# Kernel tuning notes

Hardware: AMD Instinct MI355X
Metric: run time of the kernel (lower is better)

## Reference

```python
import jax, jax.numpy as jnp
import numpy as np

B, F, L, P, H = 32, 64, 8192, 96, 8
HD = F // H
EPS_ATTN = 1e-6
EPS_REVIN = 1e-5
EPS_LN = 1e-5


def setup_inputs() -> dict:
    key = jax.random.key(0)
    ks = jax.random.split(key, 8)
    f32 = jnp.float32
    return {
        'x': jax.random.normal(ks[0], (B, F, L), dtype=f32),
        'gamma': jnp.ones((1, 1, F), dtype=f32),
        'beta': jnp.zeros((1, 1, F), dtype=f32),
        'ln_w': jnp.ones((F,), dtype=f32),
        'ln_b': jnp.zeros((F,), dtype=f32),
        'Wq': 0.05 * jax.random.normal(ks[1], (F, F), dtype=f32),
        'bq': jnp.zeros((F,), dtype=f32),
        'Wk': 0.05 * jax.random.normal(ks[2], (F, F), dtype=f32),
        'bk': jnp.zeros((F,), dtype=f32),
        'Wv': 0.05 * jax.random.normal(ks[3], (F, F), dtype=f32),
        'bv': jnp.zeros((F,), dtype=f32),
        'Wo': 0.05 * jax.random.normal(ks[4], (F, F), dtype=f32),
        'bo': jnp.zeros((F,), dtype=f32),
        'Wlin': 0.01 * jax.random.normal(ks[5], (P, L), dtype=f32),
        'blin': jnp.zeros((P,), dtype=f32),
        'Wp': 0.1 * jax.random.normal(ks[6], (1, F), dtype=f32),
        'bp': jnp.zeros((1,), dtype=f32),
    }


def _phi(t):
    # feature map: elu(x) + 1 (non-negative)
    return jax.nn.elu(t) + 1.0


def _layernorm(h, w, b):
    mu = jnp.mean(h, axis=-1, keepdims=True)
    var = jnp.mean(jnp.square(h - mu), axis=-1, keepdims=True)
    return (h - mu) * jax.lax.rsqrt(var + EPS_LN) * w + b


def reference(x, gamma, beta, ln_w, ln_b, Wq, bq, Wk, bk, Wv, bv, Wo, bo,
              Wlin, blin, Wp, bp):
    # (B, F, L) -> (B, L, F)
    xt = jnp.transpose(x, (0, 2, 1))
    # RevIN norm (stats over time axis, detached; torch std is unbiased ddof=1)
    mean = jax.lax.stop_gradient(jnp.mean(xt, axis=1, keepdims=True))
    std = jax.lax.stop_gradient(jnp.std(xt, axis=1, keepdims=True, ddof=1) + EPS_REVIN)
    xn = (xt - mean) / std * gamma + beta
    residual = xn
    h = _layernorm(xn, ln_w, ln_b)
    # Q/K/V projections (torch Linear: h @ W.T + b)
    Q = h @ Wq.T + bq
    K = h @ Wk.T + bk
    V = h @ Wv.T + bv
    # (B, L, F) -> (B, H, L, HD)
    def heads(t):
        return jnp.transpose(t.reshape(B, L, H, HD), (0, 2, 1, 3))
    Q, K, V = heads(Q), heads(K), heads(V)
    Q, K = _phi(Q), _phi(K)
    # linear attention: phi(Q) (phi(K)^T V) / (phi(Q) sum_n phi(K))
    KV = jnp.einsum('bhnd,bhne->bhde', K, V)           # (B,H,HD,HD)
    out = jnp.einsum('bhnd,bhde->bhne', Q, KV)          # (B,H,L,HD)
    Z = jnp.sum(K, axis=2)                              # (B,H,HD)
    normalizer = jnp.einsum('bhnd,bhd->bhn', Q, Z)[..., None] + EPS_ATTN
    out = out / normalizer
    out = jnp.transpose(out, (0, 2, 1, 3)).reshape(B, L, F)
    out = out @ Wo.T + bo
    y = out + residual                                  # (B, L, F)
    # temporal linear: (B, F, L) @ Wlin.T -> (B, F, P) -> (B, P, F)
    y = jnp.transpose(jnp.transpose(y, (0, 2, 1)) @ Wlin.T + blin, (0, 2, 1))
    # RevIN denorm
    y = (y - beta) / gamma
    y = y * std + mean
    # projector to scalar per step
    return (y @ Wp.T + bp)[..., 0]                      # (B, P)
```

## Files before the change

kernel.cpp:

```cpp
#include <hip/hip_runtime.h>
#include <cstddef>

#define NB 32
#define NF 64
#define NL 8192
#define NP 96
#define NH 8
#define TSPLIT 16

#define WS_MEAN 0
#define WS_STD  2048
#define WS_RSTD 4096
#define WS_KV   6144
#define WS_Z    22528
#define WS_OUT2 24576
#define WS_MUN  221184
#define WS_RSN  483328
#define WS_WLB  745472
#define WS_XNB  1138688
#define WS_YT   9527296
#define WS_WKV  17915904
#define WS_WQO  17920512
#define WS_SKT  17925120
#define WS_SQT  17925376

typedef __bf16 bfx8 __attribute__((ext_vector_type(8)));
typedef float f32x4 __attribute__((ext_vector_type(4)));
#define MFMA16(a, b, c) __builtin_amdgcn_mfma_f32_16x16x32_bf16((a), (b), (c), 0, 0, 0)

__device__ __forceinline__ unsigned short f2bf(float f) {
  unsigned u = __float_as_uint(f);
  unsigned r = u + 0x7FFFu + ((u >> 16) & 1u);
  return (unsigned short)(r >> 16);
}
__device__ __forceinline__ unsigned packbf2(float lo, float hi) {
  return (unsigned)f2bf(lo) | ((unsigned)f2bf(hi) << 16);
}
__device__ __forceinline__ float bflo(unsigned d) { return __uint_as_float(d << 16); }
__device__ __forceinline__ float bfhi(unsigned d) { return __uint_as_float(d & 0xFFFF0000u); }
__device__ __forceinline__ float bf1(unsigned short s) { return __uint_as_float(((unsigned)s) << 16); }

__device__ __forceinline__ bfx8 ldfrag(const unsigned short* p) {
  uint4 u = *(const uint4*)p;
  return __builtin_bit_cast(bfx8, u);
}

__global__ __launch_bounds__(256) void k_pre(
    const float* __restrict__ x, const float* __restrict__ Wlin,
    const float* __restrict__ lnw, const float* __restrict__ lnb,
    const float* __restrict__ Wk, const float* __restrict__ bk,
    const float* __restrict__ Wv, const float* __restrict__ bv,
    const float* __restrict__ Wq, const float* __restrict__ bq,
    const float* __restrict__ Wo,
    float* __restrict__ wmean, float* __restrict__ wstd, float* __restrict__ wrstd,
    unsigned short* __restrict__ wlb, float* __restrict__ zz,
    unsigned short* __restrict__ wWkv, unsigned short* __restrict__ wWqo,
    float* __restrict__ wSkT, float* __restrict__ wSqT) {
  __shared__ float r1[4], r2[4];
  const int bid = blockIdx.x, tid = threadIdx.x;
  if (bid < NB * NF) {
    const float4* row4 = (const float4*)(x + (size_t)bid * NL);
    float s1 = 0.f, s2 = 0.f;
#pragma unroll
    for (int i = 0; i < NL / 4 / 256; i++) {
      float4 v = row4[tid + i * 256];
      s1 += v.x + v.y + v.z + v.w;
      s2 += v.x * v.x + v.y * v.y + v.z * v.z + v.w * v.w;
    }
#pragma unroll
    for (int off = 32; off > 0; off >>= 1) {
      s1 += __shfl_down(s1, off, 64);
      s2 += __shfl_down(s2, off, 64);
    }
    if ((tid & 63) == 0) { r1[tid >> 6] = s1; r2[tid >> 6] = s2; }
    __syncthreads();
    if (tid == 0) {
      s1 = r1[0] + r1[1] + r1[2] + r1[3];
      s2 = r2[0] + r2[1] + r2[2] + r2[3];
      float m = s1 * (1.f / NL);
      float var = (s2 - (float)NL * m * m) * (1.f / (NL - 1));
      float sd = sqrtf(fmaxf(var, 0.f)) + 1e-5f;
      wmean[bid] = m;
      wstd[bid] = sd;
      wrstd[bid] = 1.f / sd;
    }
    unsigned zi = (unsigned)bid * 256u + (unsigned)tid;
    if (zi < 215040u) zz[zi] = 0.f;
  } else if (bid < NB * NF + NP * NL / 8 / 256) {
    int i = (bid - NB * NF) * 256 + tid;
    int p = i >> 10;
    int l8 = (i & 1023) * 8;
    float4 va = *(const float4*)&Wlin[(size_t)p * NL + l8];
    float4 vb = *(const float4*)&Wlin[(size_t)p * NL + l8 + 4];
    uint4 o;
    o.x = packbf2(va.x, va.y); o.y = packbf2(va.z, va.w);
    o.z = packbf2(vb.x, vb.y); o.w = packbf2(vb.z, vb.w);
    *(uint4*)&wlb[(((size_t)(l8 >> 5)) * NP + p) * 32 + (l8 & 31)] = o;
  } else if (bid == NB * NF + NP * NL / 8 / 256) {
    int jj = tid >> 2, g = tid & 3;
    int f0 = g * 16;
    float tkp = 0.f, tvp = 0.f, skp = 0.f, svp = 0.f;
#pragma unroll
    for (int i = 0; i < 4; i++) {
      int f = f0 + i * 4;
      float4 wk4 = *(const float4*)&Wk[jj * NF + f];
      float4 wv4 = *(const float4*)&Wv[jj * NF + f];
      float4 lw  = *(const float4*)&lnw[f];
      float4 lb  = *(const float4*)&lnb[f];
      uint2 pk2, pv2;
      pk2.x = packbf2(wk4.x * lw.x, wk4.y * lw.y);
      pk2.y = packbf2(wk4.z * lw.z, wk4.w * lw.w);
      pv2.x = packbf2(wv4.x * lw.x, wv4.y * lw.y);
      pv2.y = packbf2(wv4.z * lw.z, wv4.w * lw.w);
      *(uint2*)&wWkv[jj * 72 + f] = pk2;
      *(uint2*)&wWkv[4608 + jj * 72 + f] = pv2;
      tkp += lb.x * wk4.x + lb.y * wk4.y + lb.z * wk4.z + lb.w * wk4.w;
      tvp += lb.x * wv4.x + lb.y * wv4.y + lb.z * wv4.z + lb.w * wv4.w;
      skp += bflo(pk2.x) + bfhi(pk2.x) + bflo(pk2.y) + bfhi(pk2.y);
      svp += bflo(pv2.x) + bfhi(pv2.x) + bflo(pv2.y) + bfhi(pv2.y);
    }
    tkp += __shfl_xor(tkp, 1, 64); tkp += __shfl_xor(tkp, 2, 64);
    tvp += __shfl_xor(tvp, 1, 64); tvp += __shfl_xor(tvp, 2, 64);
    skp += __shfl_xor(skp, 1, 64); skp += __shfl_xor(skp, 2, 64);
    svp += __shfl_xor(svp, 1, 64); svp += __shfl_xor(svp, 2, 64);
    if (g == 0) {
      wSkT[jj]       = skp;
      wSkT[64 + jj]  = tkp + bk[jj];
      wSkT[128 + jj] = svp;
      wSkT[192 + jj] = tvp + bv[jj];
    }
  } else {
    int jj = tid >> 2, g = tid & 3;
    int f0 = g * 16;
    float tqp = 0.f, sqp = 0.f;
#pragma unroll
    for (int i = 0; i < 4; i++) {
      int f = f0 + i * 4;
      float4 wq4 = *(const float4*)&Wq[jj * NF + f];
      float4 wo4 = *(const float4*)&Wo[jj * NF + f];
      float4 lw  = *(const float4*)&lnw[f];
      float4 lb  = *(const float4*)&lnb[f];
      uint2 pq2, po2;
      pq2.x = packbf2(wq4.x * lw.x, wq4.y * lw.y);
      pq2.y = packbf2(wq4.z * lw.z, wq4.w * lw.w);
      po2.x = packbf2(wo4.x, wo4.y);
      po2.y = packbf2(wo4.z, wo4.w);
      *(uint2*)&wWqo[jj * 72 + f] = pq2;
      *(uint2*)&wWqo[4608 + jj * 72 + f] = po2;
      tqp += lb.x * wq4.x + lb.y * wq4.y + lb.z * wq4.z + lb.w * wq4.w;
      sqp += bflo(pq2.x) + bfhi(pq2.x) + bflo(pq2.y) + bfhi(pq2.y);
    }
    tqp += __shfl_xor(tqp, 1, 64); tqp += __shfl_xor(tqp, 2, 64);
    sqp += __shfl_xor(sqp, 1, 64); sqp += __shfl_xor(sqp, 2, 64);
    if (g == 0) { wSqT[jj] = sqp; wSqT[64 + jj] = tqp + bq[jj]; }
  }
}

__global__ __launch_bounds__(256, 4) void k_kv(
    const float* __restrict__ x,
    const float* __restrict__ gamma, const float* __restrict__ beta,
    const unsigned short* __restrict__ wWkv, const float* __restrict__ wSkT,
    const float* __restrict__ wmean, const float* __restrict__ wrstd,
    float* __restrict__ wKV, float* __restrict__ wZ,
    float* __restrict__ wmun, float* __restrict__ wrsn,
    unsigned short* __restrict__ xnb) {
  __shared__ __align__(16) char smem[39424];
  unsigned short* hA  = (unsigned short*)smem;
  unsigned short* WkB = (unsigned short*)(smem + 18432);
  unsigned short* WvB = (unsigned short*)(smem + 27648);
  unsigned short* pK  = (unsigned short*)smem;
  unsigned short* pV  = (unsigned short*)(smem + 17408);
  float* SkT  = (float*)(smem + 36864);
  float* mun  = (float*)(smem + 37888);
  float* rsn  = (float*)(smem + 38400);
  float* cbc  = (float*)(smem + 38912);

  const int tid = threadIdx.x;
  const int b = blockIdx.x >> 6;
  const int tI = blockIdx.x & 63;
  const int L0 = tI * 128;
  const int lane = tid & 63, wv = tid >> 6;
  const int mm = lane & 15, qd = lane >> 4;

  if (tid < 64) {
    float cb = wrstd[b * NF + tid] * gamma[tid];
    cbc[2 * tid] = cb;
    cbc[2 * tid + 1] = beta[tid] - wmean[b * NF + tid] * cb;
  }
  {
    uint4* dst = (uint4*)(smem + 18432);
    const uint4* src = (const uint4*)wWkv;
#pragma unroll
    for (int i = 0; i < 4; i++) dst[tid + i * 256] = src[tid + i * 256];
    if (tid < 128) dst[tid + 1024] = src[tid + 1024];
    SkT[tid] = wSkT[tid];
  }
  __syncthreads();

  {
    const int lt = tid >> 3;
    const int fg = tid & 7;
    const int l0q = lt * 4;
    const float* xp = x + ((size_t)(b * NF + fg * 8)) * NL + L0 + l0q;
    f32x4 v[8];
#pragma unroll
    for (int i = 0; i < 8; i++) v[i] = *(const f32x4*)(xp + (size_t)i * NL);
    float a[8][4];
#pragma unroll
    for (int i = 0; i < 4; i++) {
      float4 c = *(const float4*)&cbc[fg * 16 + i * 4];
#pragma unroll
      for (int j = 0; j < 4; j++) {
        a[2 * i][j]     = fmaf(v[2 * i][j], c.x, c.y);
        a[2 * i + 1][j] = fmaf(v[2 * i + 1][j], c.z, c.w);
      }
    }
    float s1[4], s2[4];
#pragma unroll
    for (int j = 0; j < 4; j++) {
      s1[j] = 0.f; s2[j] = 0.f;
#pragma unroll
      for (int i = 0; i < 8; i++) {
        s1[j] += a[i][j];
        s2[j] = fmaf(a[i][j], a[i][j], s2[j]);
      }
    }
#pragma unroll
    for (int m = 1; m <= 4; m <<= 1) {
#pragma unroll
      for (int j = 0; j < 4; j++) {
        s1[j] += __shfl_xor(s1[j], m, 64);
        s2[j] += __shfl_xor(s2[j], m, 64);
      }
    }
#pragma unroll
    for (int j = 0; j < 4; j++) {
      uint4 o;
      o.x = packbf2(a[0][j], a[1][j]);
      o.y = packbf2(a[2][j], a[3][j]);
      o.z = packbf2(a[4][j], a[5][j]);
      o.w = packbf2(a[6][j], a[7][j]);
      *(uint4*)&hA[(l0q + j) * 72 + fg * 8] = o;
      *(uint4*)(xnb + (((size_t)(b * 64 + tI) * 128 + l0q + j) * 64 + fg * 8)) = o;
    }
    if (fg == 0) {
      float mv[4], rv[4];
#pragma unroll
      for (int j = 0; j < 4; j++) {
        float mu = s1[j] * (1.f / NF);
        float var = s2[j] * (1.f / NF) - mu * mu;
        mv[j] = mu;
        rv[j] = rsqrtf(fmaxf(var, 0.f) + 1e-5f);
      }
      float4 m4 = {mv[0], mv[1], mv[2], mv[3]};
      float4 r4 = {rv[0], rv[1], rv[2], rv[3]};
      *(float4*)&mun[l0q] = m4;
      *(float4*)&rsn[l0q] = r4;
      *(float4*)&wmun[(size_t)b * NL + L0 + l0q] = m4;
      *(float4*)&wrsn[(size_t)b * NL + L0 + l0q] = r4;
    }
  }
  __syncthreads();

  const f32x4 fz = {0.f, 0.f, 0.f, 0.f};
  f32x4 kacc[2][4], vacc[2][4];
#pragma unroll
  for (int i = 0; i < 2; i++)
#pragma unroll
    for (int jt = 0; jt < 4; jt++) { kacc[i][jt] = fz; vacc[i][jt] = fz; }

#pragma unroll
  for (int kc = 0; kc < 2; kc++) {
    bfx8 a0 = ldfrag(&hA[(wv * 32 + mm) * 72 + kc * 32 + qd * 8]);
    bfx8 a1 = ldfrag(&hA[(wv * 32 + 16 + mm) * 72 + kc * 32 + qd * 8]);
#pragma unroll
    for (int jt = 0; jt < 4; jt++) {
      bfx8 bkf = ldfrag(&WkB[(jt * 16 + mm) * 72 + kc * 32 + qd * 8]);
      bfx8 bvf = ldfrag(&WvB[(jt * 16 + mm) * 72 + kc * 32 + qd * 8]);
      kacc[0][jt] = MFMA16(a0, bkf, kacc[0][jt]);
      kacc[1][jt] = MFMA16(a1, bkf, kacc[1][jt]);
      vacc[0][jt] = MFMA16(a0, bvf, vacc[0][jt]);
      vacc[1][jt] = MFMA16(a1, bvf, vacc[1][jt]);
    }
  }

#pragma unroll
  for (int lt2 = 0; lt2 < 2; lt2++) {
    float4 mu4 = *(const float4*)&mun[wv * 32 + lt2 * 16 + qd * 4];
    float4 rs4 = *(const float4*)&rsn[wv * 32 + lt2 * 16 + qd * 4];
    float muv[4] = {mu4.x, mu4.y, mu4.z, mu4.w};
    float rsv[4] = {rs4.x, rs4.y, rs4.z, rs4.w};
#pragma unroll
    for (int jt = 0; jt < 4; jt++) {
      int j = jt * 16 + mm;
      float Sk = SkT[j], Tk = SkT[64 + j], Sv = SkT[128 + j], Tv = SkT[192 + j];
#pragma unroll
      for (int r = 0; r < 4; r++) {
        float kk = rsv[r] * (kacc[lt2][jt][r] - muv[r] * Sk) + Tk;
        kacc[lt2][jt][r] = (kk > 0.f) ? (kk + 1.f) : __expf(kk);
        vacc[lt2][jt][r] = rsv[r] * (vacc[lt2][jt][r] - muv[r] * Sv) + Tv;
      }
    }
  }

  {
#pragma unroll
    for (int jt = 0; jt < 4; jt++) {
      float z = 0.f;
#pragma unroll
      for (int lt2 = 0; lt2 < 2; lt2++)
#pragma unroll
        for (int r = 0; r < 4; r++) z += kacc[lt2][jt][r];
      z += __shfl_xor(z, 16, 64);
      z += __shfl_xor(z, 32, 64);
      if (qd == 0) atomicAdd(&wZ[b * 64 + jt * 16 + mm], z);
    }
  }
  __syncthreads();

#pragma unroll
  for (int lt2 = 0; lt2 < 2; lt2++) {
    int l0 = wv * 32 + lt2 * 16 + qd * 4;
#pragma unroll
    for (int jt = 0; jt < 4; jt++) {
      int j = jt * 16 + mm;
      uint2 dk, dv;
      dk.x = packbf2(kacc[lt2][jt][0], kacc[lt2][jt][1]);
      dk.y = packbf2(kacc[lt2][jt][2], kacc[lt2][jt][3]);
      dv.x = packbf2(vacc[lt2][jt][0], vacc[lt2][jt][1]);
      dv.y = packbf2(vacc[lt2][jt][2], vacc[lt2][jt][3]);
      *(uint2*)&pK[j * 136 + l0] = dk;
      *(uint2*)&pV[j * 136 + l0] = dv;
    }
  }
  __syncthreads();

  {
    f32x4 racc = fz;
#pragma unroll
    for (int kb = 0; kb < 4; kb++) {
      bfx8 ak = ldfrag(&pK[(wv * 16 + mm) * 136 + kb * 32 + qd * 8]);
      bfx8 bv8 = ldfrag(&pV[(wv * 16 + mm) * 136 + kb * 32 + qd * 8]);
      racc = MFMA16(ak, bv8, racc);
    }
    int eh = mm >> 3, e = mm & 7;
#pragma unroll
    for (int r = 0; r < 4; r++) {
      int row = qd * 4 + r;
      if ((row >> 3) == eh)
        atomicAdd(&wKV[(b * NH + wv * 2 + eh) * 64 + (row & 7) * 8 + e], racc[r]);
    }
  }
}

__global__ __launch_bounds__(256, 4) void k_qy(
    const unsigned short* __restrict__ xnb,
    const unsigned short* __restrict__ wWqo, const float* __restrict__ wSqT,
    const float* __restrict__ bo,
    const float* __restrict__ wmun, const float* __restrict__ wrsn,
    const float* __restrict__ wKV, const float* __restrict__ wZ,
    unsigned short* __restrict__ ytb) {
  __shared__ __align__(16) char smem[40960];
  unsigned short* hA  = (unsigned short*)smem;
  unsigned short* qaA = (unsigned short*)smem;
  unsigned short* WqB = (unsigned short*)(smem + 18432);
  unsigned short* WoB = (unsigned short*)(smem + 27648);
  float* kvz   = (float*)(smem + 36864);
  float* mun   = (float*)(smem + 39424);
  float* rsn   = (float*)(smem + 39936);
  float* SqTq  = (float*)(smem + 40448);

  const int tid = threadIdx.x;
  const int b = blockIdx.x >> 6;
  const int tI = blockIdx.x & 63;
  const int L0 = tI * 128;
  const int lane = tid & 63, wv = tid >> 6;
  const int mm = lane & 15, qd = lane >> 4;
  const unsigned short* xtile = xnb + (size_t)(b * 64 + tI) * 128 * 64;

  {
    uint4* dst = (uint4*)(smem + 18432);
    const uint4* src = (const uint4*)wWqo;
#pragma unroll
    for (int i = 0; i < 4; i++) dst[tid + i * 256] = src[tid + i * 256];
    if (tid < 128) dst[tid + 1024] = src[tid + 1024];
    if (tid < 128) SqTq[tid] = wSqT[tid];
  }
  for (int i = tid; i < 640; i += 256)
    kvz[i] = (i < 512) ? wKV[b * 512 + i] : (i < 576 ? wZ[b * 64 + i - 512] : bo[i - 576]);
  {
    int row = tid >> 1, half = tid & 1;
    const uint4* s4 = (const uint4*)(xtile + (size_t)row * 64 + half * 32);
    uint4 u0 = s4[0], u1 = s4[1], u2 = s4[2], u3 = s4[3];
    uint4* d4 = (uint4*)&hA[row * 72 + half * 32];
    d4[0] = u0; d4[1] = u1; d4[2] = u2; d4[3] = u3;
  }
  if (tid < 64) {
    int h = tid >> 5, i = tid & 31;
    const float* src = h ? wrsn : wmun;
    float4 v = *(const float4*)&src[(size_t)b * NL + L0 + i * 4];
    *(float4*)&((h ? rsn : mun)[i * 4]) = v;
  }
  __syncthreads();

  const f32x4 fz = {0.f, 0.f, 0.f, 0.f};

  {
    f32x4 qacc[2][4];
#pragma unroll
    for (int i = 0; i < 2; i++)
#pragma unroll
      for (int jt = 0; jt < 4; jt++) qacc[i][jt] = fz;
#pragma unroll
    for (int kc = 0; kc < 2; kc++) {
      bfx8 a0 = ldfrag(&hA[(wv * 32 + mm) * 72 + kc * 32 + qd * 8]);
      bfx8 a1 = ldfrag(&hA[(wv * 32 + 16 + mm) * 72 + kc * 32 + qd * 8]);
#pragma unroll
      for (int jt = 0; jt < 4; jt++) {
        bfx8 bqf = ldfrag(&WqB[(jt * 16 + mm) * 72 + kc * 32 + qd * 8]);
        qacc[0][jt] = MFMA16(a0, bqf, qacc[0][jt]);
        qacc[1][jt] = MFMA16(a1, bqf, qacc[1][jt]);
      }
    }
#pragma unroll
    for (int lt2 = 0; lt2 < 2; lt2++) {
      float4 mu4 = *(const float4*)&mun[wv * 32 + lt2 * 16 + qd * 4];
      float4 rs4 = *(const float4*)&rsn[wv * 32 + lt2 * 16 + qd * 4];
      float muv[4] = {mu4.x, mu4.y, mu4.z, mu4.w};
      float rsv[4] = {rs4.x, rs4.y, rs4.z, rs4.w};
      int l0 = wv * 32 + lt2 * 16 + qd * 4;
#pragma unroll
      for (int jt = 0; jt < 4; jt++) {
        int j = jt * 16 + mm;
        float Sj = SqTq[j], Tj = SqTq[64 + j];
#pragma unroll
        for (int r = 0; r < 4; r++) {
          float q = rsv[r] * (qacc[lt2][jt][r] - muv[r] * Sj) + Tj;
          q = (q > 0.f) ? (q + 1.f) : __expf(q);
          qaA[(l0 + r) * 72 + j] = f2bf(q);
        }
      }
    }
  }
  __syncthreads();

  {
    int lt = tid & 31, hd = tid >> 5;
#pragma unroll
    for (int hp = 0; hp < 2; hp++) {
      int lbase = lt * 4 + hp * 2;
      float qv[2][8];
#pragma unroll
      for (int i = 0; i < 2; i++) {
        uint4 u = *(const uint4*)&qaA[(lbase + i) * 72 + hd * 8];
        qv[i][0] = bflo(u.x); qv[i][1] = bfhi(u.x);
        qv[i][2] = bflo(u.y); qv[i][3] = bfhi(u.y);
        qv[i][4] = bflo(u.z); qv[i][5] = bfhi(u.z);
        qv[i][6] = bflo(u.w); qv[i][7] = bfhi(u.w);
      }
      float att[2][8], nrm[2];
#pragma unroll
      for (int i = 0; i < 2; i++) {
        nrm[i] = 1e-6f;
#pragma unroll
        for (int e = 0; e < 8; e++) att[i][e] = 0.f;
      }
#pragma unroll
      for (int d = 0; d < 8; d++) {
        float zd = kvz[512 + hd * 8 + d];
        float4 kva = *(const float4*)&kvz[hd * 64 + d * 8];
        float4 kvb = *(const float4*)&kvz[hd * 64 + d * 8 + 4];
#pragma unroll
        for (int i = 0; i < 2; i++) {
          float qq = qv[i][d];
          nrm[i] = fmaf(qq, zd, nrm[i]);
          att[i][0] = fmaf(qq, kva.x, att[i][0]);
          att[i][1] = fmaf(qq, kva.y, att[i][1]);
          att[i][2] = fmaf(qq, kva.z, att[i][2]);
          att[i][3] = fmaf(qq, kva.w, att[i][3]);
          att[i][4] = fmaf(qq, kvb.x, att[i][4]);
          att[i][5] = fmaf(qq, kvb.y, att[i][5]);
          att[i][6] = fmaf(qq, kvb.z, att[i][6]);
          att[i][7] = fmaf(qq, kvb.w, att[i][7]);
        }
      }
#pragma unroll
      for (int i = 0; i < 2; i++) {
        float inv = 1.f / nrm[i];
        uint4 o;
        o.x = packbf2(att[i][0] * inv, att[i][1] * inv);
        o.y = packbf2(att[i][2] * inv, att[i][3] * inv);
        o.z = packbf2(att[i][4] * inv, att[i][5] * inv);
        o.w = packbf2(att[i][6] * inv, att[i][7] * inv);
        *(uint4*)&qaA[(lbase + i) * 72 + hd * 8] = o;
      }
    }
  }
  __syncthreads();

  {
    f32x4 yacc[2][4];
#pragma unroll
    for (int i = 0; i < 2; i++)
#pragma unroll
      for (int ft = 0; ft < 4; ft++) yacc[i][ft] = fz;
#pragma unroll
    for (int ec = 0; ec < 2; ec++) {
      bfx8 a0 = ldfrag(&qaA[(wv * 32 + mm) * 72 + ec * 32 + qd * 8]);
      bfx8 a1 = ldfrag(&qaA[(wv * 32 + 16 + mm) * 72 + ec * 32 + qd * 8]);
#pragma unroll
      for (int ft = 0; ft < 4; ft++) {
        bfx8 bof = ldfrag(&WoB[(ft * 16 + mm) * 72 + ec * 32 + qd * 8]);
        yacc[0][ft] = MFMA16(a0, bof, yacc[0][ft]);
        yacc[1][ft] = MFMA16(a1, bof, yacc[1][ft]);
      }
    }
#pragma unroll
    for (int lt2 = 0; lt2 < 2; lt2++) {
      int l0 = wv * 32 + lt2 * 16 + qd * 4;
#pragma unroll
      for (int ft = 0; ft < 4; ft++) {
        int ff = ft * 16 + mm;
        float bof = kvz[576 + ff];
        float v0 = yacc[lt2][ft][0] + bf1(xtile[(size_t)(l0 + 0) * 64 + ff]) + bof;
        float v1 = yacc[lt2][ft][1] + bf1(xtile[(size_t)(l0 + 1) * 64 + ff]) + bof;
        float v2 = yacc[lt2][ft][2] + bf1(xtile[(size_t)(l0 + 2) * 64 + ff]) + bof;
        float v3 = yacc[lt2][ft][3] + bf1(xtile[(size_t)(l0 + 3) * 64 + ff]) + bof;
        uint2 o2;
        o2.x = packbf2(v0, v1);
        o2.y = packbf2(v2, v3);
        size_t idx = (((size_t)b * (NL / 32) + (L0 >> 5) + wv) * 64 + ff) * 32 + lt2 * 16 + qd * 4;
        *(uint2*)&ytb[idx] = o2;
      }
    }
  }
}

__global__ __launch_bounds__(256) void k_temporal(
    const unsigned short* __restrict__ ytb, const unsigned short* __restrict__ wlb,
    float* __restrict__ out2) {
  const int tid = threadIdx.x, lane = tid & 63, wvx = tid >> 6;
  const int mm = lane & 15, qd = lane >> 4;
  const int b = blockIdx.x / TSPLIT;
  const int kc = blockIdx.x % TSPLIT;
  const f32x4 fz = {0.f, 0.f, 0.f, 0.f};
  f32x4 acc[6];
#pragma unroll
  for (int pt = 0; pt < 6; pt++) acc[pt] = fz;

#pragma unroll 2
  for (int ks = 0; ks < NL / 32 / TSPLIT; ks++) {
    int lg = kc * (NL / 32 / TSPLIT) + ks;
    bfx8 bfr = ldfrag(&ytb[(((size_t)b * (NL / 32) + lg) * 64 + wvx * 16 + mm) * 32 + qd * 8]);
#pragma unroll
    for (int pt = 0; pt < 6; pt++) {
      bfx8 afr = ldfrag(&wlb[((size_t)lg * NP + pt * 16 + mm) * 32 + qd * 8]);
      acc[pt] = MFMA16(afr, bfr, acc[pt]);
    }
  }
  const int ff = wvx * 16 + mm;
#pragma unroll
  for (int pt = 0; pt < 6; pt++) {
#pragma unroll
    for (int r = 0; r < 4; r++) {
      int p = pt * 16 + qd * 4 + r;
      atomicAdd(&out2[((size_t)(b * NP + p)) * NF + ff], acc[pt][r]);
    }
  }
}

__global__ __launch_bounds__(256) void k_final(
    const float* __restrict__ out2, const float* __restrict__ blin,
    const float* __restrict__ gamma, const float* __restrict__ beta,
    const float* __restrict__ wmean, const float* __restrict__ wstd,
    const float* __restrict__ Wp, const float* __restrict__ bp0,
    float* __restrict__ out) {
  int bp = blockIdx.x * 4 + (threadIdx.x >> 6);
  int f = threadIdx.x & 63;
  int b = bp / NP, p = bp % NP;
  float v = out2[(size_t)bp * NF + f] + blin[p];
  v = (v - beta[f]) / gamma[f];
  v = v * wstd[b * NF + f] + wmean[b * NF + f];
  float s = v * Wp[f];
#pragma unroll
  for (int off = 32; off > 0; off >>= 1)
    s += __shfl_down(s, off, 64);
  if (f == 0) out[bp] = s + bp0[0];
}

extern "C" void kernel_launch(void* const* d_in, const int* in_sizes, int n_in,
                              void* d_out, int out_size, void* d_ws, size_t ws_size,
                              hipStream_t stream) {
  const float* x     = (const float*)d_in[0];
  const float* gamma = (const float*)d_in[1];
  const float* beta  = (const float*)d_in[2];
  const float* lnw   = (const float*)d_in[3];
  const float* lnb   = (const float*)d_in[4];
  const float* Wq    = (const float*)d_in[5];
  const float* bq    = (const float*)d_in[6];
  const float* Wk    = (const float*)d_in[7];
  const float* bk    = (const float*)d_in[8];
  const float* Wv    = (const float*)d_in[9];
  const float* bv    = (const float*)d_in[10];
  const float* Wo    = (const float*)d_in[11];
  const float* bo    = (const float*)d_in[12];
  const float* Wlin  = (const float*)d_in[13];
  const float* blin  = (const float*)d_in[14];
  const float* Wp    = (const float*)d_in[15];
  const float* bp    = (const float*)d_in[16];
  float* out = (float*)d_out;
  float* ws  = (float*)d_ws;

  float* wmean = ws + WS_MEAN;
  float* wstd  = ws + WS_STD;
  float* wrstd = ws + WS_RSTD;
  float* wKV   = ws + WS_KV;
  float* wZ    = ws + WS_Z;
  float* wout2 = ws + WS_OUT2;
  float* wmun  = ws + WS_MUN;
  float* wrsn  = ws + WS_RSN;
  unsigned short* wlb = (unsigned short*)(ws + WS_WLB);
  unsigned short* xnb = (unsigned short*)(ws + WS_XNB);
  unsigned short* ytb = (unsigned short*)(ws + WS_YT);
  unsigned short* wWkv = (unsigned short*)(ws + WS_WKV);
  unsigned short* wWqo = (unsigned short*)(ws + WS_WQO);
  float* wSkT = ws + WS_SKT;
  float* wSqT = ws + WS_SQT;

  k_pre<<<NB * NF + NP * NL / 8 / 256 + 2, 256, 0, stream>>>(
      x, Wlin, lnw, lnb, Wk, bk, Wv, bv, Wq, bq, Wo,
      wmean, wstd, wrstd, wlb, wKV, wWkv, wWqo, wSkT, wSqT);
  k_kv<<<NB * 64, 256, 0, stream>>>(x, gamma, beta, wWkv, wSkT,
                                    wmean, wrstd, wKV, wZ, wmun, wrsn, xnb);
  k_qy<<<NB * 64, 256, 0, stream>>>(xnb, wWqo, wSqT, bo,
                                    wmun, wrsn, wKV, wZ, ytb);
  k_temporal<<<NB * TSPLIT, 256, 0, stream>>>(ytb, wlb, wout2);
  k_final<<<NB * NP / 4, 256, 0, stream>>>(wout2, blin, gamma, beta, wmean, wstd, Wp, bp, out);
}
```

Baseline: 211.1 us.

## Read bf16 weight fragments from global and halve K/V staging LDS

Both the k_kv and k_qy kernels stop copying the Wk/Wv and Wq/Wo bf16 weight tiles into shared memory. MFMA B-fragments are now loaded straight from global memory, where the small weights should stay in cache. In k_kv the K/V transpose staging is split into two halves, with each wave pair writing in turn and extra barriers between them, which roughly halves LDS per block. The aim is higher occupancy and no cooperative weight copy, at the cost of more global/L2 fragment loads and extra synchronisation in the KV reduction.

```diff
diff --git a/kernel.cpp b/kernel.cpp
--- a/kernel.cpp
+++ b/kernel.cpp
@@ -164,16 +164,14 @@
     float* __restrict__ wKV, float* __restrict__ wZ,
     float* __restrict__ wmun, float* __restrict__ wrsn,
     unsigned short* __restrict__ xnb) {
-  __shared__ __align__(16) char smem[39424];
+  __shared__ __align__(16) char smem[20992];
   unsigned short* hA  = (unsigned short*)smem;
-  unsigned short* WkB = (unsigned short*)(smem + 18432);
-  unsigned short* WvB = (unsigned short*)(smem + 27648);
-  unsigned short* pK  = (unsigned short*)smem;
-  unsigned short* pV  = (unsigned short*)(smem + 17408);
-  float* SkT  = (float*)(smem + 36864);
-  float* mun  = (float*)(smem + 37888);
-  float* rsn  = (float*)(smem + 38400);
-  float* cbc  = (float*)(smem + 38912);
+  unsigned short* pKh = (unsigned short*)smem;
+  unsigned short* pVh = (unsigned short*)(smem + 9216);
+  float* SkT = (float*)(smem + 18432);
+  float* mun = (float*)(smem + 19456);
+  float* rsn = (float*)(smem + 19968);
+  float* cbc = (float*)(smem + 20480);
 
   const int tid = threadIdx.x;
   const int b = blockIdx.x >> 6;
@@ -187,14 +185,7 @@
     cbc[2 * tid] = cb;
     cbc[2 * tid + 1] = beta[tid] - wmean[b * NF + tid] * cb;
   }
-  {
-    uint4* dst = (uint4*)(smem + 18432);
-    const uint4* src = (const uint4*)wWkv;
-#pragma unroll
-    for (int i = 0; i < 4; i++) dst[tid + i * 256] = src[tid + i * 256];
-    if (tid < 128) dst[tid + 1024] = src[tid + 1024];
-    SkT[tid] = wSkT[tid];
-  }
+  SkT[tid] = wSkT[tid];
   __syncthreads();
 
   {
@@ -275,8 +266,8 @@
     bfx8 a1 = ldfrag(&hA[(wv * 32 + 16 + mm) * 72 + kc * 32 + qd * 8]);
 #pragma unroll
     for (int jt = 0; jt < 4; jt++) {
-      bfx8 bkf = ldfrag(&WkB[(jt * 16 + mm) * 72 + kc * 32 + qd * 8]);
-      bfx8 bvf = ldfrag(&WvB[(jt * 16 + mm) * 72 + kc * 32 + qd * 8]);
+      bfx8 bkf = ldfrag(&wWkv[(jt * 16 + mm) * 72 + kc * 32 + qd * 8]);
+      bfx8 bvf = ldfrag(&wWkv[4608 + (jt * 16 + mm) * 72 + kc * 32 + qd * 8]);
       kacc[0][jt] = MFMA16(a0, bkf, kacc[0][jt]);
       kacc[1][jt] = MFMA16(a1, bkf, kacc[1][jt]);
       vacc[0][jt] = MFMA16(a0, bvf, vacc[0][jt]);
@@ -316,32 +307,36 @@
       if (qd == 0) atomicAdd(&wZ[b * 64 + jt * 16 + mm], z);
     }
   }
-  __syncthreads();
-
-#pragma unroll
-  for (int lt2 = 0; lt2 < 2; lt2++) {
-    int l0 = wv * 32 + lt2 * 16 + qd * 4;
-#pragma unroll
-    for (int jt = 0; jt < 4; jt++) {
-      int j = jt * 16 + mm;
-      uint2 dk, dv;
-      dk.x = packbf2(kacc[lt2][jt][0], kacc[lt2][jt][1]);
-      dk.y = packbf2(kacc[lt2][jt][2], kacc[lt2][jt][3]);
-      dv.x = packbf2(vacc[lt2][jt][0], vacc[lt2][jt][1]);
-      dv.y = packbf2(vacc[lt2][jt][2], vacc[lt2][jt][3]);
-      *(uint2*)&pK[j * 136 + l0] = dk;
-      *(uint2*)&pV[j * 136 + l0] = dv;
-    }
-  }
-  __syncthreads();
 
   {
     f32x4 racc = fz;
 #pragma unroll
-    for (int kb = 0; kb < 4; kb++) {
-      bfx8 ak = ldfrag(&pK[(wv * 16 + mm) * 136 + kb * 32 + qd * 8]);
-      bfx8 bv8 = ldfrag(&pV[(wv * 16 + mm) * 136 + kb * 32 + qd * 8]);
-      racc = MFMA16(ak, bv8, racc);
+    for (int h = 0; h < 2; h++) {
+      __syncthreads();
+      if ((wv >> 1) == h) {
+#pragma unroll
+        for (int lt2 = 0; lt2 < 2; lt2++) {
+          int lcol = (wv & 1) * 32 + lt2 * 16 + qd * 4;
+#pragma unroll
+          for (int jt = 0; jt < 4; jt++) {
+            int j = jt * 16 + mm;
+            uint2 dk, dv;
+            dk.x = packbf2(kacc[lt2][jt][0], kacc[lt2][jt][1]);
+            dk.y = packbf2(kacc[lt2][jt][2], kacc[lt2][jt][3]);
+            dv.x = packbf2(vacc[lt2][jt][0], vacc[lt2][jt][1]);
+            dv.y = packbf2(vacc[lt2][jt][2], vacc[lt2][jt][3]);
+            *(uint2*)&pKh[j * 72 + lcol] = dk;
+            *(uint2*)&pVh[j * 72 + lcol] = dv;
+          }
+        }
+      }
+      __syncthreads();
+#pragma unroll
+      for (int kb = 0; kb < 2; kb++) {
+        bfx8 ak  = ldfrag(&pKh[(wv * 16 + mm) * 72 + kb * 32 + qd * 8]);
+        bfx8 bv8 = ldfrag(&pVh[(wv * 16 + mm) * 72 + kb * 32 + qd * 8]);
+        racc = MFMA16(ak, bv8, racc);
+      }
     }
     int eh = mm >> 3, e = mm & 7;
 #pragma unroll
@@ -360,15 +355,13 @@
     const float* __restrict__ wmun, const float* __restrict__ wrsn,
     const float* __restrict__ wKV, const float* __restrict__ wZ,
     unsigned short* __restrict__ ytb) {
-  __shared__ __align__(16) char smem[40960];
+  __shared__ __align__(16) char smem[22528];
   unsigned short* hA  = (unsigned short*)smem;
   unsigned short* qaA = (unsigned short*)smem;
-  unsigned short* WqB = (unsigned short*)(smem + 18432);
-  unsigned short* WoB = (unsigned short*)(smem + 27648);
-  float* kvz   = (float*)(smem + 36864);
-  float* mun   = (float*)(smem + 39424);
-  float* rsn   = (float*)(smem + 39936);
-  float* SqTq  = (float*)(smem + 40448);
+  float* kvz  = (float*)(smem + 18432);
+  float* mun  = (float*)(smem + 20992);
+  float* rsn  = (float*)(smem + 21504);
+  float* SqTq = (float*)(smem + 22016);
 
   const int tid = threadIdx.x;
   const int b = blockIdx.x >> 6;
@@ -378,16 +371,9 @@
   const int mm = lane & 15, qd = lane >> 4;
   const unsigned short* xtile = xnb + (size_t)(b * 64 + tI) * 128 * 64;
 
-  {
-    uint4* dst = (uint4*)(smem + 18432);
-    const uint4* src = (const uint4*)wWqo;
-#pragma unroll
-    for (int i = 0; i < 4; i++) dst[tid + i * 256] = src[tid + i * 256];
-    if (tid < 128) dst[tid + 1024] = src[tid + 1024];
-    if (tid < 128) SqTq[tid] = wSqT[tid];
-  }
   for (int i = tid; i < 640; i += 256)
     kvz[i] = (i < 512) ? wKV[b * 512 + i] : (i < 576 ? wZ[b * 64 + i - 512] : bo[i - 576]);
+  if (tid < 128) SqTq[tid] = wSqT[tid];
   {
     int row = tid >> 1, half = tid & 1;
     const uint4* s4 = (const uint4*)(xtile + (size_t)row * 64 + half * 32);
@@ -417,7 +403,7 @@
       bfx8 a1 = ldfrag(&hA[(wv * 32 + 16 + mm) * 72 + kc * 32 + qd * 8]);
 #pragma unroll
       for (int jt = 0; jt < 4; jt++) {
-        bfx8 bqf = ldfrag(&WqB[(jt * 16 + mm) * 72 + kc * 32 + qd * 8]);
+        bfx8 bqf = ldfrag(&wWqo[(jt * 16 + mm) * 72 + kc * 32 + qd * 8]);
         qacc[0][jt] = MFMA16(a0, bqf, qacc[0][jt]);
         qacc[1][jt] = MFMA16(a1, bqf, qacc[1][jt]);
       }
@@ -510,7 +496,7 @@
       bfx8 a1 = ldfrag(&qaA[(wv * 32 + 16 + mm) * 72 + ec * 32 + qd * 8]);
 #pragma unroll
       for (int ft = 0; ft < 4; ft++) {
-        bfx8 bof = ldfrag(&WoB[(ft * 16 + mm) * 72 + ec * 32 + qd * 8]);
+        bfx8 bof = ldfrag(&wWqo[4608 + (ft * 16 + mm) * 72 + ec * 32 + qd * 8]);
         yacc[0][ft] = MFMA16(a0, bof, yacc[0][ft]);
         yacc[1][ft] = MFMA16(a1, bof, yacc[1][ft]);
       }
```

New measurement: 212.3 us. Within noise of the previous version (+0.5%).
